# Optimization experiments

Measured on AMD Instinct MI355X. Metric: run time of the kernel, lower is better.

## Reference

```python
import jax, jax.numpy as jnp
import numpy as np

N, E = 50000, 800000
IN_F, OUT_F, H = 128, 128, 4
D = OUT_F // H  # head dim
NEG_SLOPE = 0.2
EPS = 1e-12


def setup_inputs() -> dict:
    key = jax.random.key(0)
    ks = jax.random.split(key, 10)
    s = 1.0 / np.sqrt(IN_F)
    return {
        "x": jax.random.normal(ks[0], (N, IN_F), jnp.float32),
        "W_src": jax.random.normal(ks[1], (IN_F, H * D), jnp.float32) * s,
        "b_src": jnp.zeros((H * D,), jnp.float32),
        "W_dst": jax.random.normal(ks[2], (IN_F, H * D), jnp.float32) * s,
        "b_dst": jnp.zeros((H * D,), jnp.float32),
        "attn": jax.random.normal(ks[3], (H, D), jnp.float32) * (1.0 / np.sqrt(D)),
        "out_bias": jnp.zeros((H * D,), jnp.float32),
        "ln_w": jnp.ones((OUT_F,), jnp.float32),
        "ln_b": jnp.zeros((OUT_F,), jnp.float32),
        "src": jax.random.randint(ks[4], (E,), 0, N, jnp.int32),
        "dst": jax.random.randint(ks[5], (E,), 0, N, jnp.int32),
    }


def reference(x, W_src, b_src, W_dst, b_dst, attn, out_bias, ln_w, ln_b, src, dst):
    n = x.shape[0]
    # GATv2Conv (share_weights=False): separate source/dest projections
    fs = (x @ W_src + b_src).reshape(n, H, D)  # [N,H,D]
    fd = (x @ W_dst + b_dst).reshape(n, H, D)
    # per-edge scores: e_ij = attn . leaky_relu(fs[u] + fd[v])
    e = jax.nn.leaky_relu(fs[src] + fd[dst], NEG_SLOPE)  # [E,H,D]
    logits = jnp.einsum("ehd,hd->eh", e, attn)  # [E,H]
    # edge softmax over incoming edges of each dst node
    m = jax.ops.segment_max(logits, dst, num_segments=n)  # [N,H]
    ex = jnp.exp(logits - m[dst])
    denom = jax.ops.segment_sum(ex, dst, num_segments=n)  # [N,H]
    alpha = ex / denom[dst]  # [E,H]
    # aggregate: sum_j alpha_ij * fs[j]
    msg = alpha[:, :, None] * fs[src]  # [E,H,D]
    rst = jax.ops.segment_sum(msg, dst, num_segments=n)  # [N,H,D]
    h = rst.reshape(n, H * D) + out_bias
    # LayerNorm (biased variance, eps inside sqrt)
    u = h.mean(-1, keepdims=True)
    s = jnp.mean((h - u) ** 2, -1, keepdims=True)
    h = (h - u) / jnp.sqrt(s + EPS)
    h = ln_w * h + ln_b
    # activation = elu; dropout p=0 -> identity
    return jax.nn.elu(h)
```

## Files before the change

### kernel.cpp

```cpp
#include <hip/hip_runtime.h>
#include <hip/hip_bf16.h>

constexpr int NF = 128;

using bf16x8 = __attribute__((ext_vector_type(8))) short;
using f32x4v = __attribute__((ext_vector_type(4))) float;

__device__ __forceinline__ unsigned short f2bs(float f) {
    return __builtin_bit_cast(unsigned short, __float2bfloat16(f));
}
__device__ __forceinline__ void unpack8(float4 raw, float* a) {
    unsigned u0 = __float_as_uint(raw.x);
    unsigned u1 = __float_as_uint(raw.y);
    unsigned u2 = __float_as_uint(raw.z);
    unsigned u3 = __float_as_uint(raw.w);
    a[0] = __uint_as_float(u0 << 16);
    a[1] = __uint_as_float(u0 & 0xffff0000u);
    a[2] = __uint_as_float(u1 << 16);
    a[3] = __uint_as_float(u1 & 0xffff0000u);
    a[4] = __uint_as_float(u2 << 16);
    a[5] = __uint_as_float(u2 & 0xffff0000u);
    a[6] = __uint_as_float(u3 << 16);
    a[7] = __uint_as_float(u3 & 0xffff0000u);
}

__global__ void GraphAttnLayer_70196945486348_kernel() {}

__global__ __launch_bounds__(256) void prep_kernel(
    const float* __restrict__ Wsrc, const float* __restrict__ Wdst,
    unsigned short* __restrict__ Wb,
    int* __restrict__ cnt, int* __restrict__ state, int N, int NB)
{
    int i = blockIdx.x * 256 + threadIdx.x;
    if (i < N) cnt[i] = 0;
    if (i < NB) state[i] = 0;
    if (i < 256 * NF) {
        int k   = i >> 8;
        int col = i & 255;
        float v = (col < 128) ? Wsrc[k * NF + col] : Wdst[k * NF + (col - 128)];
        Wb[col * NF + k] = f2bs(v);
    }
}

__global__ __launch_bounds__(256) void gemm_hist_kernel(
    const float* __restrict__ x,
    const unsigned short* __restrict__ Wb,
    const float* __restrict__ bsrc, const float* __restrict__ bdst,
    unsigned short* __restrict__ fs,
    float* __restrict__ fd,
    const int* __restrict__ src, const int* __restrict__ dst,
    int* __restrict__ cnt, int* __restrict__ pack,
    int N, int E, int NGB)
{
    {
        int e = blockIdx.x * 256 + threadIdx.x;
        if (e < E) {
            int r = atomicAdd(&cnt[dst[e]], 1);
            pack[e] = (r << 17) | src[e];
        }
    }
    if (blockIdx.x >= NGB) return;

    const int lane = threadIdx.x & 63;
    const int wave = threadIdx.x >> 6;
    const int m_base = blockIdx.x * 32;
    const int lm = lane & 15;
    const int kq = (lane >> 4) * 8;

    bf16x8 bfrag[4][4];
    float bias[4];
#pragma unroll
    for (int c = 0; c < 4; ++c) {
        int col = wave * 64 + c * 16 + lm;
        bias[c] = (col < 128) ? bsrc[col] : bdst[col - 128];
#pragma unroll
        for (int s = 0; s < 4; ++s)
            bfrag[c][s] = *(const bf16x8*)(Wb + col * NF + s * 32 + kq);
    }

    for (int r = 0; r < 2; ++r) {
        int m0 = m_base + r * 16;
        if (m0 >= N) break;
        int row = m0 + lm;
        if (row >= N) row = N - 1;
        bf16x8 afrag[4];
#pragma unroll
        for (int s = 0; s < 4; ++s) {
            const float4* xp = (const float4*)(x + (size_t)row * NF + s * 32 + kq);
            float4 xa = xp[0], xb = xp[1];
            afrag[s][0] = (short)f2bs(xa.x);
            afrag[s][1] = (short)f2bs(xa.y);
            afrag[s][2] = (short)f2bs(xa.z);
            afrag[s][3] = (short)f2bs(xa.w);
            afrag[s][4] = (short)f2bs(xb.x);
            afrag[s][5] = (short)f2bs(xb.y);
            afrag[s][6] = (short)f2bs(xb.z);
            afrag[s][7] = (short)f2bs(xb.w);
        }
#pragma unroll
        for (int c = 0; c < 4; ++c) {
            f32x4v acc = {0.f, 0.f, 0.f, 0.f};
#pragma unroll
            for (int s = 0; s < 4; ++s)
                acc = __builtin_amdgcn_mfma_f32_16x16x32_bf16(afrag[s], bfrag[c][s], acc, 0, 0, 0);
            int col = wave * 64 + c * 16 + lm;
            int cc = col & 127;
#pragma unroll
            for (int rr = 0; rr < 4; ++rr) {
                int rowd = m0 + (lane >> 4) * 4 + rr;
                if (rowd < N) {
                    float v = acc[rr] + bias[c];
                    if (col < 128) fs[(size_t)rowd * NF + cc] = f2bs(v);
                    else           fd[(size_t)rowd * NF + cc] = v;
                }
            }
        }
    }
}

__global__ __launch_bounds__(256) void scan_kernel(
    const int* __restrict__ cnt, int* __restrict__ rowptr,
    int* __restrict__ state, int N, int E)
{
    int b = blockIdx.x, t = threadIdx.x;
    int i = b * 256 + t;
    int v = (i < N) ? cnt[i] : 0;

    __shared__ int arr[256];
    __shared__ int s_bofs;
    arr[t] = v;
    __syncthreads();
    for (int off = 1; off < 256; off <<= 1) {
        int u = (t >= off) ? arr[t - off] : 0;
        __syncthreads();
        arr[t] += u;
        __syncthreads();
    }
    int total = arr[255];

    if (t < 64) {
        if (t == 0) {
            int word = ((b == 0 ? 2 : 1) << 30) | total;
            atomicExch(&state[b], word);
        }
        int bofs = 0;
        if (b > 0) {
            int base = b;
            for (;;) {
                int j = base - 1 - t;
                int sv = 0, f = 1;
                if (j >= 0) {
                    sv = atomicAdd(&state[j], 0);
                    f = ((unsigned)sv) >> 30;
                }
                unsigned long long notready = __ballot(f == 0);
                if (notready) continue;
                unsigned long long has2 = __ballot(f == 2);
                if (has2) {
                    int k = (int)(__ffsll((unsigned long long)has2) - 1);
                    int val = (t <= k) ? (sv & 0x3FFFFFFF) : 0;
#pragma unroll
                    for (int off = 32; off; off >>= 1) val += __shfl_xor(val, off);
                    bofs += val;
                    break;
                } else {
                    int val = (j >= 0) ? (sv & 0x3FFFFFFF) : 0;
#pragma unroll
                    for (int off = 32; off; off >>= 1) val += __shfl_xor(val, off);
                    bofs += val;
                    base -= 64;
                }
            }
            if (t == 0) atomicExch(&state[b], (2 << 30) | (bofs + total));
        }
        if (t == 0) s_bofs = bofs;
    }
    __syncthreads();
    int bofs = s_bofs;
    int excl = arr[t] - v + bofs;
    if (i < N) rowptr[i] = excl;
    if (i == 0) rowptr[N] = E;
}

__global__ __launch_bounds__(256) void scatter_kernel(
    const int* __restrict__ dst, const int* __restrict__ pack,
    const int* __restrict__ rowptr, int* __restrict__ src_sorted, int E)
{
    int idx = blockIdx.x * 256 + threadIdx.x;
    int e0 = idx * 4;
    if (e0 + 3 < E) {
        int4 d = *(const int4*)(dst + e0);
        int4 p = *(const int4*)(pack + e0);
        src_sorted[rowptr[d.x] + (p.x >> 17)] = p.x & 0x1FFFF;
        src_sorted[rowptr[d.y] + (p.y >> 17)] = p.y & 0x1FFFF;
        src_sorted[rowptr[d.z] + (p.z >> 17)] = p.z & 0x1FFFF;
        src_sorted[rowptr[d.w] + (p.w >> 17)] = p.w & 0x1FFFF;
    } else {
        for (int e = e0; e < E; ++e) {
            int p = pack[e];
            src_sorted[rowptr[dst[e]] + (p >> 17)] = p & 0x1FFFF;
        }
    }
}

__global__ __launch_bounds__(256) void node_kernel(
    const float4* __restrict__ fsq,
    const int* __restrict__ rowptr, const int* __restrict__ src_sorted,
    const float4* __restrict__ attn4,
    const float4* __restrict__ obias4,
    const float4* __restrict__ lnw4,
    const float4* __restrict__ lnb4,
    float4* __restrict__ out4, int N)
{
    int lane = threadIdx.x & 63;
    int es = lane >> 4;
    int g  = lane & 15;
    int n = blockIdx.x * 4 + (threadIdx.x >> 6);
    if (n >= N) return;

    float4 fda = out4[(size_t)n * 32 + g * 2];
    float4 fdb = out4[(size_t)n * 32 + g * 2 + 1];
    float4 ava = attn4[g * 2];
    float4 avb = attn4[g * 2 + 1];
    float fd[8] = {fda.x, fda.y, fda.z, fda.w, fdb.x, fdb.y, fdb.z, fdb.w};
    float av[8] = {ava.x, ava.y, ava.z, ava.w, avb.x, avb.y, avb.z, avb.w};

    int beg = rowptr[n], end = rowptr[n + 1];
    float l = 0.f;
    float ac[8] = {0.f, 0.f, 0.f, 0.f, 0.f, 0.f, 0.f, 0.f};

    for (int j = beg; j < end; j += 4) {
        int idx = j + es;
        bool valid = idx < end;
        int s = src_sorted[valid ? idx : (end - 1)];
        float4 raw = fsq[(size_t)s * 16 + g];
        float a[8];
        unpack8(raw, a);
        float p = 0.f;
#pragma unroll
        for (int d = 0; d < 8; ++d) {
            float t = a[d] + fd[d];
            t = fmaxf(t, 0.2f * t);
            p += av[d] * t;
        }
        p += __shfl_xor(p, 1);
        p += __shfl_xor(p, 2);
        float e = valid ? __expf(p) : 0.f;
        l += e;
#pragma unroll
        for (int d = 0; d < 8; ++d) ac[d] += e * a[d];
    }

    l += __shfl_xor(l, 16);
    l += __shfl_xor(l, 32);
#pragma unroll
    for (int d = 0; d < 8; ++d) {
        ac[d] += __shfl_xor(ac[d], 16);
        ac[d] += __shfl_xor(ac[d], 32);
    }

    float rl = (l > 0.f) ? (1.f / l) : 0.f;
    float4 oba = obias4[g * 2];
    float4 obb = obias4[g * 2 + 1];
    float ob[8] = {oba.x, oba.y, oba.z, oba.w, obb.x, obb.y, obb.z, obb.w};
    float h[8];
    float s1 = 0.f, s2 = 0.f;
#pragma unroll
    for (int d = 0; d < 8; ++d) {
        h[d] = ac[d] * rl + ob[d];
        s1 += h[d];
        s2 += h[d] * h[d];
    }
    s1 += __shfl_xor(s1, 1); s2 += __shfl_xor(s2, 1);
    s1 += __shfl_xor(s1, 2); s2 += __shfl_xor(s2, 2);
    s1 += __shfl_xor(s1, 4); s2 += __shfl_xor(s2, 4);
    s1 += __shfl_xor(s1, 8); s2 += __shfl_xor(s2, 8);

    float u = s1 * (1.f / NF);
    float var = s2 * (1.f / NF) - u * u;
    float rstd = rsqrtf(fmaxf(var, 0.f) + 1e-12f);
    float4 gwa = lnw4[g * 2], gwb = lnw4[g * 2 + 1];
    float4 gba = lnb4[g * 2], gbb = lnb4[g * 2 + 1];
    float gw[8] = {gwa.x, gwa.y, gwa.z, gwa.w, gwb.x, gwb.y, gwb.z, gwb.w};
    float gb[8] = {gba.x, gba.y, gba.z, gba.w, gbb.x, gbb.y, gbb.z, gbb.w};
    float z[8];
#pragma unroll
    for (int d = 0; d < 8; ++d) {
        float y = gw[d] * ((h[d] - u) * rstd) + gb[d];
        z[d] = (y > 0.f) ? y : (__expf(y) - 1.f);
    }
    if (es == 0) {
        out4[(size_t)n * 32 + g * 2]     = make_float4(z[0], z[1], z[2], z[3]);
        out4[(size_t)n * 32 + g * 2 + 1] = make_float4(z[4], z[5], z[6], z[7]);
    }
}

extern "C" void kernel_launch(void* const* d_in, const int* in_sizes, int n_in,
                              void* d_out, int out_size, void* d_ws, size_t ws_size,
                              hipStream_t stream)
{
    const float* x    = (const float*)d_in[0];
    const float* Wsrc = (const float*)d_in[1];
    const float* bsrc = (const float*)d_in[2];
    const float* Wdst = (const float*)d_in[3];
    const float* bdst = (const float*)d_in[4];
    const float4* attn4 = (const float4*)d_in[5];
    const float4* obias4= (const float4*)d_in[6];
    const float4* lnw4  = (const float4*)d_in[7];
    const float4* lnb4  = (const float4*)d_in[8];
    const int* src = (const int*)d_in[9];
    const int* dst = (const int*)d_in[10];
    int N = in_sizes[0] / NF;
    int E = in_sizes[9];
    int NB = (N + 255) / 256;

    int* cnt = (int*)d_ws;
    int* rowptr = cnt + N;
    int* state = rowptr + (N + 1);
    int* pack = state + NB;
    int* srcs = pack + E;
    unsigned short* Wb = (unsigned short*)(srcs + E);
    unsigned short* fs = Wb + 256 * NF;

    int NGB = (N + 31) / 32;
    int GB  = (E + 255) / 256;
    if (GB < NGB) GB = NGB;

    prep_kernel<<<NB, 256, 0, stream>>>(Wsrc, Wdst, Wb, cnt, state, N, NB);
    gemm_hist_kernel<<<GB, 256, 0, stream>>>(
        x, Wb, bsrc, bdst, fs, (float*)d_out, src, dst, cnt, pack, N, E, NGB);
    scan_kernel<<<NB, 256, 0, stream>>>(cnt, rowptr, state, N, E);
    scatter_kernel<<<(E / 4 + 255) / 256, 256, 0, stream>>>(dst, pack, rowptr, srcs, E);
    node_kernel<<<(N + 3) / 4, 256, 0, stream>>>(
        (const float4*)fs, rowptr, srcs, attn4, obias4, lnw4, lnb4,
        (float4*)d_out, N);
}
```

Measured before the change: 212.6 us.

## Fuse scan and scatter into one kernel with grid barrier; use 16-bit source indices

Merges the decoupled-lookback scan and the CSR scatter into a single launch. Every block spins on a global done counter until all scan blocks have finished, then performs the scatter. The sorted source indices are also shrunk from int to unsigned short, with the rank packed into the upper 16 bits, to cut scatter writes and node-kernel gather bytes. The grid-wide spin barrier assumes all scan blocks are co-resident or run first, which is a deadlock risk. The 16-bit packing only holds while N and the per-node in-degree stay below 65536.

```diff
diff --git a/kernel.cpp b/kernel.cpp
--- a/kernel.cpp
+++ b/kernel.cpp
@@ -29,11 +29,13 @@
 __global__ __launch_bounds__(256) void prep_kernel(
     const float* __restrict__ Wsrc, const float* __restrict__ Wdst,
     unsigned short* __restrict__ Wb,
-    int* __restrict__ cnt, int* __restrict__ state, int N, int NB)
+    int* __restrict__ cnt, int* __restrict__ state, int* __restrict__ done,
+    int N, int NB)
 {
     int i = blockIdx.x * 256 + threadIdx.x;
     if (i < N) cnt[i] = 0;
     if (i < NB) state[i] = 0;
+    if (i == 0) *done = 0;
     if (i < 256 * NF) {
         int k   = i >> 8;
         int col = i & 255;
@@ -56,7 +58,7 @@
         int e = blockIdx.x * 256 + threadIdx.x;
         if (e < E) {
             int r = atomicAdd(&cnt[dst[e]], 1);
-            pack[e] = (r << 17) | src[e];
+            pack[e] = (r << 16) | src[e];
         }
     }
     if (blockIdx.x >= NGB) return;
@@ -118,94 +120,107 @@
     }
 }
 
-__global__ __launch_bounds__(256) void scan_kernel(
+__global__ __launch_bounds__(256) void scan_scatter_kernel(
     const int* __restrict__ cnt, int* __restrict__ rowptr,
-    int* __restrict__ state, int N, int E)
+    int* __restrict__ state, int* __restrict__ done,
+    const int* __restrict__ dst, const int* __restrict__ pack,
+    unsigned short* __restrict__ src_sorted,
+    int N, int E, int NB)
 {
     int b = blockIdx.x, t = threadIdx.x;
-    int i = b * 256 + t;
-    int v = (i < N) ? cnt[i] : 0;
-
-    __shared__ int arr[256];
-    __shared__ int s_bofs;
-    arr[t] = v;
+
+    if (b < NB) {
+        int i = b * 256 + t;
+        int v = (i < N) ? cnt[i] : 0;
+
+        __shared__ int arr[256];
+        __shared__ int s_bofs;
+        arr[t] = v;
+        __syncthreads();
+        for (int off = 1; off < 256; off <<= 1) {
+            int u = (t >= off) ? arr[t - off] : 0;
+            __syncthreads();
+            arr[t] += u;
+            __syncthreads();
+        }
+        int total = arr[255];
+
+        if (t < 64) {
+            if (t == 0) {
+                int word = ((b == 0 ? 2 : 1) << 30) | total;
+                atomicExch(&state[b], word);
+            }
+            int bofs = 0;
+            if (b > 0) {
+                int base = b;
+                for (;;) {
+                    int j = base - 1 - t;
+                    int sv = 0, f = 1;
+                    if (j >= 0) {
+                        sv = __hip_atomic_load(&state[j], __ATOMIC_RELAXED,
+                                               __HIP_MEMORY_SCOPE_AGENT);
+                        f = ((unsigned)sv) >> 30;
+                    }
+                    unsigned long long notready = __ballot(f == 0);
+                    if (notready) continue;
+                    unsigned long long has2 = __ballot(f == 2);
+                    if (has2) {
+                        int k = (int)(__ffsll((unsigned long long)has2) - 1);
+                        int val = (t <= k) ? (sv & 0x3FFFFFFF) : 0;
+#pragma unroll
+                        for (int off = 32; off; off >>= 1) val += __shfl_xor(val, off);
+                        bofs += val;
+                        break;
+                    } else {
+                        int val = (j >= 0) ? (sv & 0x3FFFFFFF) : 0;
+#pragma unroll
+                        for (int off = 32; off; off >>= 1) val += __shfl_xor(val, off);
+                        bofs += val;
+                        base -= 64;
+                    }
+                }
+                if (t == 0) atomicExch(&state[b], (2 << 30) | (bofs + total));
+            }
+            if (t == 0) s_bofs = bofs;
+        }
+        __syncthreads();
+        int bofs = s_bofs;
+        int excl = arr[t] - v + bofs;
+        if (i < N) rowptr[i] = excl;
+        if (i == 0) rowptr[N] = E;
+        __syncthreads();
+        if (t == 0) {
+            __threadfence();
+            atomicAdd(done, 1);
+        }
+    }
+
+    if (t == 0) {
+        while (__hip_atomic_load(done, __ATOMIC_ACQUIRE,
+                                 __HIP_MEMORY_SCOPE_AGENT) < NB) {}
+    }
     __syncthreads();
-    for (int off = 1; off < 256; off <<= 1) {
-        int u = (t >= off) ? arr[t - off] : 0;
-        __syncthreads();
-        arr[t] += u;
-        __syncthreads();
-    }
-    int total = arr[255];
-
-    if (t < 64) {
-        if (t == 0) {
-            int word = ((b == 0 ? 2 : 1) << 30) | total;
-            atomicExch(&state[b], word);
-        }
-        int bofs = 0;
-        if (b > 0) {
-            int base = b;
-            for (;;) {
-                int j = base - 1 - t;
-                int sv = 0, f = 1;
-                if (j >= 0) {
-                    sv = atomicAdd(&state[j], 0);
-                    f = ((unsigned)sv) >> 30;
-                }
-                unsigned long long notready = __ballot(f == 0);
-                if (notready) continue;
-                unsigned long long has2 = __ballot(f == 2);
-                if (has2) {
-                    int k = (int)(__ffsll((unsigned long long)has2) - 1);
-                    int val = (t <= k) ? (sv & 0x3FFFFFFF) : 0;
-#pragma unroll
-                    for (int off = 32; off; off >>= 1) val += __shfl_xor(val, off);
-                    bofs += val;
-                    break;
-                } else {
-                    int val = (j >= 0) ? (sv & 0x3FFFFFFF) : 0;
-#pragma unroll
-                    for (int off = 32; off; off >>= 1) val += __shfl_xor(val, off);
-                    bofs += val;
-                    base -= 64;
-                }
-            }
-            if (t == 0) atomicExch(&state[b], (2 << 30) | (bofs + total));
-        }
-        if (t == 0) s_bofs = bofs;
-    }
-    __syncthreads();
-    int bofs = s_bofs;
-    int excl = arr[t] - v + bofs;
-    if (i < N) rowptr[i] = excl;
-    if (i == 0) rowptr[N] = E;
-}
-
-__global__ __launch_bounds__(256) void scatter_kernel(
-    const int* __restrict__ dst, const int* __restrict__ pack,
-    const int* __restrict__ rowptr, int* __restrict__ src_sorted, int E)
-{
-    int idx = blockIdx.x * 256 + threadIdx.x;
+
+    int idx = b * 256 + t;
     int e0 = idx * 4;
     if (e0 + 3 < E) {
         int4 d = *(const int4*)(dst + e0);
         int4 p = *(const int4*)(pack + e0);
-        src_sorted[rowptr[d.x] + (p.x >> 17)] = p.x & 0x1FFFF;
-        src_sorted[rowptr[d.y] + (p.y >> 17)] = p.y & 0x1FFFF;
-        src_sorted[rowptr[d.z] + (p.z >> 17)] = p.z & 0x1FFFF;
-        src_sorted[rowptr[d.w] + (p.w >> 17)] = p.w & 0x1FFFF;
+        src_sorted[rowptr[d.x] + ((unsigned)p.x >> 16)] = (unsigned short)(p.x & 0xFFFF);
+        src_sorted[rowptr[d.y] + ((unsigned)p.y >> 16)] = (unsigned short)(p.y & 0xFFFF);
+        src_sorted[rowptr[d.z] + ((unsigned)p.z >> 16)] = (unsigned short)(p.z & 0xFFFF);
+        src_sorted[rowptr[d.w] + ((unsigned)p.w >> 16)] = (unsigned short)(p.w & 0xFFFF);
     } else {
         for (int e = e0; e < E; ++e) {
             int p = pack[e];
-            src_sorted[rowptr[dst[e]] + (p >> 17)] = p & 0x1FFFF;
+            src_sorted[rowptr[dst[e]] + ((unsigned)p >> 16)] = (unsigned short)(p & 0xFFFF);
         }
     }
 }
 
 __global__ __launch_bounds__(256) void node_kernel(
     const float4* __restrict__ fsq,
-    const int* __restrict__ rowptr, const int* __restrict__ src_sorted,
+    const int* __restrict__ rowptr, const unsigned short* __restrict__ src_sorted,
     const float4* __restrict__ attn4,
     const float4* __restrict__ obias4,
     const float4* __restrict__ lnw4,
@@ -315,22 +330,25 @@
     int NB = (N + 255) / 256;
 
     int* cnt = (int*)d_ws;
-    int* rowptr = cnt + N;
-    int* state = rowptr + (N + 1);
-    int* pack = state + NB;
-    int* srcs = pack + E;
-    unsigned short* Wb = (unsigned short*)(srcs + E);
+    int* state = cnt + N;
+    int* done = state + NB;
+    int* rowptr = done + 1;
+    int* pack = rowptr + (N + 1);
+    unsigned short* srcs = (unsigned short*)(pack + E);
+    unsigned short* Wb = srcs + ((E + 1) & ~1);
     unsigned short* fs = Wb + 256 * NF;
 
     int NGB = (N + 31) / 32;
     int GB  = (E + 255) / 256;
     if (GB < NGB) GB = NGB;
-
-    prep_kernel<<<NB, 256, 0, stream>>>(Wsrc, Wdst, Wb, cnt, state, N, NB);
+    int SSB = (E / 4 + 255) / 256;
+    if (SSB < NB) SSB = NB;
+
+    prep_kernel<<<NB, 256, 0, stream>>>(Wsrc, Wdst, Wb, cnt, state, done, N, NB);
     gemm_hist_kernel<<<GB, 256, 0, stream>>>(
         x, Wb, bsrc, bdst, fs, (float*)d_out, src, dst, cnt, pack, N, E, NGB);
-    scan_kernel<<<NB, 256, 0, stream>>>(cnt, rowptr, state, N, E);
-    scatter_kernel<<<(E / 4 + 255) / 256, 256, 0, stream>>>(dst, pack, rowptr, srcs, E);
+    scan_scatter_kernel<<<SSB, 256, 0, stream>>>(
+        cnt, rowptr, state, done, dst, pack, srcs, N, E, NB);
     node_kernel<<<(N + 3) / 4, 256, 0, stream>>>(
         (const float4*)fs, rowptr, srcs, attn4, obias4, lnw4, lnb4,
         (float4*)d_out, N);
```

New measurement: 253.2 us. 19.1% more time.

## Replace global-atomic counting sort with two-level LDS bucket sort of edges

Applied to the files above, without the earlier changes.

Builds the CSR by destination in a new way. Edges are first histogrammed per chunk into 256-node buckets using shared-memory atomics, and the bucket-by-chunk counts are scanned. Edges are then scattered into bucket segments, and each bucket is sorted locally in LDS to produce rowptr and the sorted sources. This replaces per-edge global atomics on random destinations with shared-memory atomics and more coalesced writes. Source indices are stored as 16-bit values, which limits N to 65536 and relies on each bucket fitting in the 16K-entry LDS buffer. It adds one extra kernel launch.

```diff
diff --git a/kernel.cpp b/kernel.cpp
--- a/kernel.cpp
+++ b/kernel.cpp
@@ -29,11 +29,10 @@
 __global__ __launch_bounds__(256) void prep_kernel(
     const float* __restrict__ Wsrc, const float* __restrict__ Wdst,
     unsigned short* __restrict__ Wb,
-    int* __restrict__ cnt, int* __restrict__ state, int N, int NB)
+    int* __restrict__ state, int NSB)
 {
     int i = blockIdx.x * 256 + threadIdx.x;
-    if (i < N) cnt[i] = 0;
-    if (i < NB) state[i] = 0;
+    if (i < NSB) state[i] = 0;
     if (i < 256 * NF) {
         int k   = i >> 8;
         int col = i & 255;
@@ -48,22 +47,29 @@
     const float* __restrict__ bsrc, const float* __restrict__ bdst,
     unsigned short* __restrict__ fs,
     float* __restrict__ fd,
-    const int* __restrict__ src, const int* __restrict__ dst,
-    int* __restrict__ cnt, int* __restrict__ pack,
-    int N, int E, int NGB)
-{
-    {
-        int e = blockIdx.x * 256 + threadIdx.x;
-        if (e < E) {
-            int r = atomicAdd(&cnt[dst[e]], 1);
-            pack[e] = (r << 17) | src[e];
-        }
-    }
-    if (blockIdx.x >= NGB) return;
-
-    const int lane = threadIdx.x & 63;
-    const int wave = threadIdx.x >> 6;
+    const int* __restrict__ dst,
+    int* __restrict__ cntT,
+    int N, int E, int C, int B)
+{
+    __shared__ int lh[256];
+    const int t = threadIdx.x;
+    if (blockIdx.x < C) {
+        lh[t] = 0;
+        __syncthreads();
+        int e0 = blockIdx.x * 4096;
+#pragma unroll
+        for (int j = 0; j < 16; ++j) {
+            int e = e0 + j * 256 + t;
+            if (e < E) atomicAdd(&lh[dst[e] >> 8], 1);
+        }
+        __syncthreads();
+        if (t < B) cntT[t * C + blockIdx.x] = lh[t];
+    }
+
+    const int lane = t & 63;
+    const int wave = t >> 6;
     const int m_base = blockIdx.x * 32;
+    if (m_base >= N) return;
     const int lm = lane & 15;
     const int kq = (lane >> 4) * 8;
 
@@ -119,12 +125,12 @@
 }
 
 __global__ __launch_bounds__(256) void scan_kernel(
-    const int* __restrict__ cnt, int* __restrict__ rowptr,
-    int* __restrict__ state, int N, int E)
+    const int* __restrict__ cntT, int* __restrict__ baseBC,
+    int* __restrict__ state, int M)
 {
     int b = blockIdx.x, t = threadIdx.x;
     int i = b * 256 + t;
-    int v = (i < N) ? cnt[i] : 0;
+    int v = (i < M) ? cntT[i] : 0;
 
     __shared__ int arr[256];
     __shared__ int s_bofs;
@@ -150,7 +156,8 @@
                 int j = base - 1 - t;
                 int sv = 0, f = 1;
                 if (j >= 0) {
-                    sv = atomicAdd(&state[j], 0);
+                    sv = __hip_atomic_load(&state[j], __ATOMIC_RELAXED,
+                                           __HIP_MEMORY_SCOPE_AGENT);
                     f = ((unsigned)sv) >> 30;
                 }
                 unsigned long long notready = __ballot(f == 0);
@@ -176,36 +183,80 @@
         if (t == 0) s_bofs = bofs;
     }
     __syncthreads();
-    int bofs = s_bofs;
-    int excl = arr[t] - v + bofs;
-    if (i < N) rowptr[i] = excl;
-    if (i == 0) rowptr[N] = E;
-}
-
-__global__ __launch_bounds__(256) void scatter_kernel(
-    const int* __restrict__ dst, const int* __restrict__ pack,
-    const int* __restrict__ rowptr, int* __restrict__ src_sorted, int E)
-{
-    int idx = blockIdx.x * 256 + threadIdx.x;
-    int e0 = idx * 4;
-    if (e0 + 3 < E) {
-        int4 d = *(const int4*)(dst + e0);
-        int4 p = *(const int4*)(pack + e0);
-        src_sorted[rowptr[d.x] + (p.x >> 17)] = p.x & 0x1FFFF;
-        src_sorted[rowptr[d.y] + (p.y >> 17)] = p.y & 0x1FFFF;
-        src_sorted[rowptr[d.z] + (p.z >> 17)] = p.z & 0x1FFFF;
-        src_sorted[rowptr[d.w] + (p.w >> 17)] = p.w & 0x1FFFF;
-    } else {
-        for (int e = e0; e < E; ++e) {
-            int p = pack[e];
-            src_sorted[rowptr[dst[e]] + (p >> 17)] = p & 0x1FFFF;
-        }
-    }
+    int excl = arr[t] - v + s_bofs;
+    if (i < M) baseBC[i] = excl;
+}
+
+__global__ __launch_bounds__(256) void scatter_pairs_kernel(
+    const int* __restrict__ dst, const int* __restrict__ src,
+    const int* __restrict__ baseBC, unsigned* __restrict__ pairs,
+    int E, int C, int B)
+{
+    __shared__ int base_lds[256];
+    __shared__ int lcnt[256];
+    int chunk = blockIdx.x, t = threadIdx.x;
+    if (t < B) base_lds[t] = baseBC[t * C + chunk];
+    lcnt[t] = 0;
+    __syncthreads();
+    int e0 = chunk * 4096;
+#pragma unroll
+    for (int j = 0; j < 16; ++j) {
+        int e = e0 + j * 256 + t;
+        if (e < E) {
+            int d = dst[e];
+            int b = d >> 8;
+            int r = atomicAdd(&lcnt[b], 1);
+            pairs[base_lds[b] + r] = ((unsigned)(d & 255) << 16) | (unsigned)src[e];
+        }
+    }
+}
+
+__global__ __launch_bounds__(256) void bucket_sort_kernel(
+    const unsigned* __restrict__ pairs, const int* __restrict__ baseBC,
+    int* __restrict__ rowptr, unsigned short* __restrict__ src_sorted,
+    int N, int E, int C, int B)
+{
+    __shared__ int h[256];
+    __shared__ int arr[256];
+    __shared__ int cur[256];
+    __shared__ unsigned short sorted[16384];
+    int b = blockIdx.x, t = threadIdx.x;
+    int segbase = baseBC[b * C];
+    int end = (b + 1 < B) ? baseBC[(b + 1) * C] : E;
+    int count = end - segbase;
+
+    h[t] = 0;
+    __syncthreads();
+    for (int i = t; i < count; i += 256)
+        atomicAdd(&h[pairs[segbase + i] >> 16], 1);
+    __syncthreads();
+    int v = h[t];
+    arr[t] = v;
+    __syncthreads();
+    for (int off = 1; off < 256; off <<= 1) {
+        int u = (t >= off) ? arr[t - off] : 0;
+        __syncthreads();
+        arr[t] += u;
+        __syncthreads();
+    }
+    int excl = arr[t] - v;
+    int node = b * 256 + t;
+    if (node <= N) rowptr[node] = segbase + excl;
+    cur[t] = excl;
+    __syncthreads();
+    for (int i = t; i < count; i += 256) {
+        unsigned p = pairs[segbase + i];
+        int r = atomicAdd(&cur[p >> 16], 1);
+        sorted[r] = (unsigned short)(p & 0xFFFF);
+    }
+    __syncthreads();
+    for (int i = t; i < count; i += 256)
+        src_sorted[segbase + i] = sorted[i];
 }
 
 __global__ __launch_bounds__(256) void node_kernel(
     const float4* __restrict__ fsq,
-    const int* __restrict__ rowptr, const int* __restrict__ src_sorted,
+    const int* __restrict__ rowptr, const unsigned short* __restrict__ src_sorted,
     const float4* __restrict__ attn4,
     const float4* __restrict__ obias4,
     const float4* __restrict__ lnw4,
@@ -312,25 +363,30 @@
     const int* dst = (const int*)d_in[10];
     int N = in_sizes[0] / NF;
     int E = in_sizes[9];
-    int NB = (N + 255) / 256;
-
-    int* cnt = (int*)d_ws;
-    int* rowptr = cnt + N;
-    int* state = rowptr + (N + 1);
-    int* pack = state + NB;
-    int* srcs = pack + E;
-    unsigned short* Wb = (unsigned short*)(srcs + E);
+
+    int C = (E + 4095) / 4096;
+    int B = (N + 255) / 256;
+    int M = B * C;
+    int NSB = (M + 255) / 256;
+
+    int* cntT = (int*)d_ws;
+    int* baseBC = cntT + M;
+    int* state = baseBC + M;
+    int* rowptr = state + 256;
+    unsigned* pairs = (unsigned*)(rowptr + (N + 1));
+    unsigned short* srcs = (unsigned short*)(pairs + E);
+    unsigned short* Wb = srcs + ((E + 1) & ~1);
     unsigned short* fs = Wb + 256 * NF;
 
     int NGB = (N + 31) / 32;
-    int GB  = (E + 255) / 256;
-    if (GB < NGB) GB = NGB;
-
-    prep_kernel<<<NB, 256, 0, stream>>>(Wsrc, Wdst, Wb, cnt, state, N, NB);
-    gemm_hist_kernel<<<GB, 256, 0, stream>>>(
-        x, Wb, bsrc, bdst, fs, (float*)d_out, src, dst, cnt, pack, N, E, NGB);
-    scan_kernel<<<NB, 256, 0, stream>>>(cnt, rowptr, state, N, E);
-    scatter_kernel<<<(E / 4 + 255) / 256, 256, 0, stream>>>(dst, pack, rowptr, srcs, E);
+    if (NGB < C) NGB = C;
+
+    prep_kernel<<<B, 256, 0, stream>>>(Wsrc, Wdst, Wb, state, NSB);
+    gemm_hist_kernel<<<NGB, 256, 0, stream>>>(
+        x, Wb, bsrc, bdst, fs, (float*)d_out, dst, cntT, N, E, C, B);
+    scan_kernel<<<NSB, 256, 0, stream>>>(cntT, baseBC, state, M);
+    scatter_pairs_kernel<<<C, 256, 0, stream>>>(dst, src, baseBC, pairs, E, C, B);
+    bucket_sort_kernel<<<B, 256, 0, stream>>>(pairs, baseBC, rowptr, srcs, N, E, C, B);
     node_kernel<<<(N + 3) / 4, 256, 0, stream>>>(
         (const float4*)fs, rowptr, srcs, attn4, obias4, lnw4, lnb4,
         (float4*)d_out, N);
```

Result: no change. 208.8 us (-1.8%).
